# Kernel tuning notes

Hardware: AMD Instinct MI355X
Metric: run time of the kernel (lower is better)

The kernel has to match this reference:

```python
import jax, jax.numpy as jnp
import numpy as np

N = 100000      # nodes
E = 1600000     # edges (before self-loops)
F_IN = 128      # num_features
H = 4           # heads
C = 32          # out_channels per head (num_hidden)
SLOPE = 0.2     # leaky relu negative slope (alpha)


def setup_inputs() -> dict:
    key = jax.random.key(0)
    k = jax.random.split(key, 6)
    x = jax.random.normal(k[0], (N, F_IN), jnp.float32)
    edge_index = jax.random.randint(k[1], (2, E), 0, N, dtype=jnp.int64)
    W = jax.random.normal(k[2], (F_IN, H * C), jnp.float32) * (1.0 / np.sqrt(F_IN))
    att_src = jax.random.normal(k[3], (H, C), jnp.float32) * 0.1
    att_dst = jax.random.normal(k[4], (H, C), jnp.float32) * 0.1
    bias = jnp.zeros((H * C,), jnp.float32)
    return dict(x=x, W=W, att_src=att_src, att_dst=att_dst, bias=bias,
                edge_index=edge_index)


def reference(x, W, att_src, att_dst, bias, edge_index):
    # PyG GATConv (concat=True, add_self_loops=True), eval mode (dropout off).
    loops = jnp.arange(N, dtype=edge_index.dtype)
    ei = jnp.concatenate([edge_index, jnp.stack([loops, loops])], axis=1)
    src, dst = ei[0], ei[1]                     # [E+N]

    h = (x @ W).reshape(N, H, C)                # projected node features
    a_src = jnp.einsum('nhc,hc->nh', h, att_src)   # [N, H]
    a_dst = jnp.einsum('nhc,hc->nh', h, att_dst)   # [N, H]

    e = a_src[src] + a_dst[dst]                 # [E+N, H]
    e = jnp.where(e > 0, e, SLOPE * e)          # leaky relu

    # segment softmax over incoming edges of each dst node (per head)
    m = jax.lax.stop_gradient(jax.ops.segment_max(e, dst, num_segments=N))
    p = jnp.exp(e - m[dst])
    denom = jax.ops.segment_sum(p, dst, num_segments=N)
    alpha = p / (denom[dst] + 1e-16)            # [E+N, H]

    # weighted scatter-aggregate of source features
    out = jax.ops.segment_sum(alpha[:, :, None] * h[src], dst, num_segments=N)
    return out.reshape(N, H * C) + bias
```

## Files before the change

kernel.cpp:

```cpp
#include <hip/hip_runtime.h>
#include <hip/hip_bf16.h>
#include <math.h>

#define N_NODES 100000
#define F_IN    128
#define HC      128
#define NH      4
#define SLOPE   0.2f

#define PADK    136

#define NB      196
#define BSH     9
#define CAP     10240
#define CHUNK   2048
#define CURPAD  16

typedef __attribute__((ext_vector_type(8))) short short8;
typedef __attribute__((ext_vector_type(4))) float f32x4;
typedef __attribute__((ext_vector_type(2))) float fx2;

static __device__ __forceinline__ float leaky(float x) { return x > 0.f ? x : SLOPE * x; }

static __device__ __forceinline__ short f2bs(float f) {
    __hip_bfloat16 b = __float2bfloat16(f);
    return *reinterpret_cast<short*>(&b);
}

__global__ __launch_bounds__(256) void k_prep(const float* __restrict__ W,
                                              unsigned short* __restrict__ wt)
{
    int t = blockIdx.x * 256 + threadIdx.x;
    if (t < 128 * 128) {
        int k = t >> 7, n = t & 127;
        wt[n * 128 + k] = (unsigned short)f2bs(W[k * HC + n]);
    }
}

__global__ __launch_bounds__(256) void k_gemm(const float* __restrict__ x,
                                              const unsigned short* __restrict__ wt,
                                              const float* __restrict__ att_src,
                                              const float* __restrict__ att_dst,
                                              unsigned short* __restrict__ hb,
                                              float* __restrict__ a_src,
                                              float* __restrict__ a_dst)
{
    __shared__ short xs[64 * PADK];
    __shared__ short ws[128 * PADK];
    const int t  = threadIdx.x;
    const int r0 = blockIdx.x * 64;

    for (int i = t; i < 2048; i += 256) {
        int row = i >> 5, kq = (i & 31) * 4;
        int gr = r0 + row;
        float4 v = make_float4(0.f, 0.f, 0.f, 0.f);
        if (gr < N_NODES) v = ((const float4*)(x + (size_t)gr * F_IN))[i & 31];
        short* p = &xs[row * PADK + kq];
        p[0] = f2bs(v.x); p[1] = f2bs(v.y); p[2] = f2bs(v.z); p[3] = f2bs(v.w);
    }
    for (int i = t; i < 2048; i += 256) {
        int n = i >> 4, k0 = (i & 15) * 8;
        *(float4*)&ws[n * PADK + k0] = *(const float4*)&wt[n * 128 + k0];
    }
    __syncthreads();

    const int wave = t >> 6, lane = t & 63;
    const int quad = lane >> 4, l16 = lane & 15;
    const int wrow = wave * 16;

    f32x4 acc[8];
    #pragma unroll
    for (int nt = 0; nt < 8; ++nt) acc[nt] = (f32x4){0.f, 0.f, 0.f, 0.f};

    const short* ap = &xs[(wrow + l16) * PADK + quad * 8];
    #pragma unroll
    for (int kb = 0; kb < 4; ++kb) {
        short8 a = *(const short8*)(ap + kb * 32);
        #pragma unroll
        for (int nt = 0; nt < 8; ++nt) {
            short8 b = *(const short8*)&ws[(nt * 16 + l16) * PADK + kb * 32 + quad * 8];
            acc[nt] = __builtin_amdgcn_mfma_f32_16x16x32_bf16(a, b, acc[nt], 0, 0, 0);
        }
    }

    float att_s[8], att_d[8];
    #pragma unroll
    for (int nt = 0; nt < 8; ++nt) {
        att_s[nt] = att_src[nt * 16 + l16];
        att_d[nt] = att_dst[nt * 16 + l16];
    }

    #pragma unroll
    for (int g = 0; g < 4; ++g) {
        int r = r0 + wrow + quad * 4 + g;
        if (r < N_NODES) {
            #pragma unroll
            for (int nt = 0; nt < 8; ++nt)
                hb[(size_t)r * HC + nt * 16 + l16] = (unsigned short)f2bs(acc[nt][g]);
        }
        float s0 = acc[0][g] * att_s[0] + acc[1][g] * att_s[1];
        float s1 = acc[2][g] * att_s[2] + acc[3][g] * att_s[3];
        float s2 = acc[4][g] * att_s[4] + acc[5][g] * att_s[5];
        float s3 = acc[6][g] * att_s[6] + acc[7][g] * att_s[7];
        float d0 = acc[0][g] * att_d[0] + acc[1][g] * att_d[1];
        float d1 = acc[2][g] * att_d[2] + acc[3][g] * att_d[3];
        float d2 = acc[4][g] * att_d[4] + acc[5][g] * att_d[5];
        float d3 = acc[6][g] * att_d[6] + acc[7][g] * att_d[7];
        #pragma unroll
        for (int o = 1; o < 16; o <<= 1) {
            s0 += __shfl_xor(s0, o); s1 += __shfl_xor(s1, o);
            s2 += __shfl_xor(s2, o); s3 += __shfl_xor(s3, o);
            d0 += __shfl_xor(d0, o); d1 += __shfl_xor(d1, o);
            d2 += __shfl_xor(d2, o); d3 += __shfl_xor(d3, o);
        }
        if (l16 == 0 && r < N_NODES) {
            *(float4*)&a_src[r * NH] = make_float4(s0, s1, s2, s3);
            *(float4*)&a_dst[r * NH] = make_float4(d0, d1, d2, d3);
        }
    }
}

__global__ __launch_bounds__(256) void k_bucket(const int* __restrict__ srcp,
                                                const int* __restrict__ dstp,
                                                int* __restrict__ bucket_cursor,
                                                int* __restrict__ eb, int E)
{
    __shared__ int ebuf[CHUNK];
    __shared__ unsigned char bkt[CHUNK];
    __shared__ int hist[256];
    __shared__ int lexcl[257];
    __shared__ int gbase[256];
    __shared__ int sdata[256];

    const int t = threadIdx.x;
    const int base = blockIdx.x * CHUNK;

    hist[t] = 0;
    __syncthreads();

    #pragma unroll
    for (int j = 0; j < CHUNK / 256; ++j) {
        int i = base + t + j * 256;
        if (i < E) atomicAdd(&hist[dstp[i] >> BSH], 1);
    }
    __syncthreads();

    int cnt = hist[t];
    sdata[t] = cnt;
    __syncthreads();
    for (int o = 1; o < 256; o <<= 1) {
        int add = (t >= o) ? sdata[t - o] : 0;
        __syncthreads();
        sdata[t] += add;
        __syncthreads();
    }
    int excl = sdata[t] - cnt;
    lexcl[t] = excl;
    if (t == 255) lexcl[256] = sdata[255];
    hist[t] = excl;
    int gb = 0;
    if (t < NB && cnt > 0) gb = atomicAdd(&bucket_cursor[t * CURPAD], cnt);
    gbase[t] = t * CAP + gb;
    __syncthreads();

    #pragma unroll
    for (int j = 0; j < CHUNK / 256; ++j) {
        int i = base + t + j * 256;
        if (i < E) {
            int s = srcp[i], d = dstp[i];
            int b = d >> BSH;
            int r = atomicAdd(&hist[b], 1);
            ebuf[r] = (s << BSH) | (d & 511);
            bkt[r] = (unsigned char)b;
        }
    }
    __syncthreads();

    const int blockTotal = lexcl[256];
    for (int i = t; i < blockTotal; i += 256) {
        int b = bkt[i];
        eb[gbase[b] + (i - lexcl[b])] = ebuf[i];
    }
}

__global__ void k_bscan(const int* __restrict__ bucket_cursor,
                        int* __restrict__ bexcl)
{
    __shared__ int sdata[256];
    const int t = threadIdx.x;
    int nvalid = 0;
    if (t < NB) {
        int n0 = t * 512;
        nvalid = min(512, N_NODES - n0);
        if (nvalid < 0) nvalid = 0;
    }
    int v = (t < NB) ? bucket_cursor[t * CURPAD] + nvalid : 0;
    sdata[t] = v;
    __syncthreads();
    for (int o = 1; o < 256; o <<= 1) {
        int add = (t >= o) ? sdata[t - o] : 0;
        __syncthreads();
        sdata[t] += add;
        __syncthreads();
    }
    if (t < NB) bexcl[t] = sdata[t] - v;
}

__global__ __launch_bounds__(1024) void k_csr(const int* __restrict__ eb,
                                              const int* __restrict__ bucket_cursor,
                                              const int* __restrict__ bexcl,
                                              int* __restrict__ col,
                                              int2* __restrict__ rowse)
{
    __shared__ int deg[512];
    __shared__ int sdata[256];

    const int t  = threadIdx.x;
    const int b  = blockIdx.x;
    const int n0 = b * 512;
    const int cnt   = bucket_cursor[b * CURPAD];
    const int ebase = b * CAP;
    const int gofs  = bexcl[b];

    if (t < 512) deg[t] = (n0 + t < N_NODES) ? 1 : 0;
    __syncthreads();

    for (int i = t; i < cnt; i += 1024)
        atomicAdd(&deg[eb[ebase + i] & 511], 1);
    __syncthreads();

    int d0 = 0, d1 = 0, ps = 0;
    if (t < 256) {
        d0 = deg[2 * t]; d1 = deg[2 * t + 1];
        ps = d0 + d1;
        sdata[t] = ps;
    }
    __syncthreads();
    for (int o = 1; o < 256; o <<= 1) {
        int add = 0;
        if (t < 256 && t >= o) add = sdata[t - o];
        __syncthreads();
        if (t < 256) sdata[t] += add;
        __syncthreads();
    }
    if (t < 256) {
        int e0 = sdata[t] - ps;
        int e1 = e0 + d0;
        int na = n0 + 2 * t, nb2 = n0 + 2 * t + 1;
        if (na < N_NODES) {
            rowse[na] = make_int2(gofs + e0, gofs + e0 + d0);
            col[gofs + e0] = na;
        }
        if (nb2 < N_NODES) {
            rowse[nb2] = make_int2(gofs + e1, gofs + e1 + d1);
            col[gofs + e1] = nb2;
        }
        deg[2 * t]     = e0 + 1;
        deg[2 * t + 1] = e1 + 1;
    }
    __syncthreads();

    for (int i = t; i < cnt; i += 1024) {
        int v = eb[ebase + i];
        int r = atomicAdd(&deg[v & 511], 1);
        col[gofs + r] = v >> BSH;
    }
}

__global__ __launch_bounds__(256) void k_node(const unsigned short* __restrict__ hb,
                                              const float* __restrict__ a_src,
                                              const float* __restrict__ a_dst,
                                              const int2* __restrict__ rowse,
                                              const int* __restrict__ col,
                                              const float* __restrict__ bias,
                                              float* __restrict__ out)
{
    const int lane = threadIdx.x & 63;
    const int node = blockIdx.x * 4 + (threadIdx.x >> 6);
    if (node >= N_NODES) return;

    const int2 se = rowse[node];
    const int r0 = se.x, r1 = se.y;
    const int myh = lane >> 4;
    const float adm = a_dst[node * NH + myh];

    float denom = 0.f, acc0 = 0.f, acc1 = 0.f;
    int i = r0;
    for (; i + 8 <= r1; i += 8) {
        int s[8];
        #pragma unroll
        for (int j = 0; j < 8; ++j) s[j] = col[i + j];
        float as[8];
        #pragma unroll
        for (int j = 0; j < 8; ++j) as[j] = a_src[s[j] * NH + myh];
        unsigned int hv[8];
        #pragma unroll
        for (int j = 0; j < 8; ++j)
            hv[j] = *(const unsigned int*)&hb[(size_t)s[j] * HC + 2 * lane];
        #pragma unroll
        for (int j = 0; j < 8; ++j) {
            float p = __expf(leaky(as[j] + adm));
            denom += p;
            acc0 += p * __uint_as_float(hv[j] << 16);
            acc1 += p * __uint_as_float(hv[j] & 0xffff0000u);
        }
    }
    for (; i < r1; ++i) {
        int s = col[i];
        float p = __expf(leaky(a_src[s * NH + myh] + adm));
        unsigned int v = *(const unsigned int*)&hb[(size_t)s * HC + 2 * lane];
        denom += p;
        acc0 += p * __uint_as_float(v << 16);
        acc1 += p * __uint_as_float(v & 0xffff0000u);
    }

    float inv = 1.f / (denom + 1e-16f);
    fx2 o2;
    o2.x = acc0 * inv + bias[2 * lane];
    o2.y = acc1 * inv + bias[2 * lane + 1];
    __builtin_nontemporal_store(o2, (fx2*)&out[(size_t)node * HC + 2 * lane]);
}

extern "C" void kernel_launch(void* const* d_in, const int* in_sizes, int n_in,
                              void* d_out, int out_size, void* d_ws, size_t ws_size,
                              hipStream_t stream)
{
    const float* x       = (const float*)d_in[0];
    const float* W       = (const float*)d_in[1];
    const float* att_src = (const float*)d_in[2];
    const float* att_dst = (const float*)d_in[3];
    const float* bias    = (const float*)d_in[4];
    const int*   ei      = (const int*)d_in[5];
    const int E = in_sizes[5] / 2;
    const int* srcp = ei;
    const int* dstp = ei + E;
    float* out = (float*)d_out;

    char* wsb = (char*)d_ws;
    size_t off = 0;
    auto alloc = [&](size_t bytes) -> char* {
        char* p = wsb + off;
        off += (bytes + 255) & ~(size_t)255;
        return p;
    };
    unsigned short* hb = (unsigned short*)alloc((size_t)N_NODES * HC * sizeof(unsigned short));
    float* a_src   = (float*)alloc((size_t)N_NODES * NH * sizeof(float));
    float* a_dst   = (float*)alloc((size_t)N_NODES * NH * sizeof(float));
    int*   eb      = (int*)alloc((size_t)NB * CAP * sizeof(int));
    int*   col     = (int*)alloc((size_t)(E + N_NODES) * sizeof(int));
    int2*  rowse   = (int2*)alloc((size_t)N_NODES * sizeof(int2));
    int*   bcursor = (int*)alloc((size_t)NB * CURPAD * sizeof(int));
    int*   bexcl   = (int*)alloc(256 * sizeof(int));
    unsigned short* wt = (unsigned short*)alloc(128 * 128 * sizeof(unsigned short));

    (void)hipMemsetAsync(bcursor, 0, (size_t)NB * CURPAD * sizeof(int), stream);

    k_prep<<<64, 256, 0, stream>>>(W, wt);
    k_gemm<<<(N_NODES + 63) / 64, 256, 0, stream>>>(x, wt, att_src, att_dst,
                                                    hb, a_src, a_dst);
    k_bucket<<<(E + CHUNK - 1) / CHUNK, 256, 0, stream>>>(srcp, dstp, bcursor, eb, E);
    k_bscan<<<1, 256, 0, stream>>>(bcursor, bexcl);
    k_csr<<<NB, 1024, 0, stream>>>(eb, bcursor, bexcl, col, rowse);
    k_node<<<(N_NODES + 3) / 4, 256, 0, stream>>>(hb, a_src, a_dst, rowse, col, bias, out);
}
```

Before: 265.8 us.

## Merge GEMM and edge-bucketing kernels, drop memset and bucket scan

Result: faster. 251.0 us (-5.6%).

```diff
diff --git a/kernel.cpp b/kernel.cpp
--- a/kernel.cpp
+++ b/kernel.cpp
@@ -13,8 +13,11 @@
 #define NB      196
 #define BSH     9
 #define CAP     10240
+#define CAPC    10752
 #define CHUNK   2048
 #define CURPAD  16
+
+#define GEMM_BLOCKS 1563
 
 typedef __attribute__((ext_vector_type(8))) short short8;
 typedef __attribute__((ext_vector_type(4))) float f32x4;
@@ -27,188 +30,173 @@
     return *reinterpret_cast<short*>(&b);
 }
 
-__global__ __launch_bounds__(256) void k_prep(const float* __restrict__ W,
-                                              unsigned short* __restrict__ wt)
+__global__ __launch_bounds__(256) void k_pre(const float* __restrict__ W,
+                                             unsigned short* __restrict__ wt,
+                                             int* __restrict__ bucket_cursor)
 {
     int t = blockIdx.x * 256 + threadIdx.x;
     if (t < 128 * 128) {
         int k = t >> 7, n = t & 127;
         wt[n * 128 + k] = (unsigned short)f2bs(W[k * HC + n]);
     }
-}
-
-__global__ __launch_bounds__(256) void k_gemm(const float* __restrict__ x,
+    if (t < NB * CURPAD) bucket_cursor[t] = 0;
+}
+
+union SMem {
+    struct {
+        short xs[64 * PADK];
+        short ws[128 * PADK];
+    } g;
+    struct {
+        int ebuf[CHUNK];
+        unsigned char bkt[CHUNK];
+        int hist[256];
+        int lexcl[257];
+        int gbase[256];
+        int sdata[256];
+    } b;
+};
+
+__global__ __launch_bounds__(256) void k_main(const float* __restrict__ x,
                                               const unsigned short* __restrict__ wt,
                                               const float* __restrict__ att_src,
                                               const float* __restrict__ att_dst,
                                               unsigned short* __restrict__ hb,
                                               float* __restrict__ a_src,
-                                              float* __restrict__ a_dst)
-{
-    __shared__ short xs[64 * PADK];
-    __shared__ short ws[128 * PADK];
-    const int t  = threadIdx.x;
-    const int r0 = blockIdx.x * 64;
-
-    for (int i = t; i < 2048; i += 256) {
-        int row = i >> 5, kq = (i & 31) * 4;
-        int gr = r0 + row;
-        float4 v = make_float4(0.f, 0.f, 0.f, 0.f);
-        if (gr < N_NODES) v = ((const float4*)(x + (size_t)gr * F_IN))[i & 31];
-        short* p = &xs[row * PADK + kq];
-        p[0] = f2bs(v.x); p[1] = f2bs(v.y); p[2] = f2bs(v.z); p[3] = f2bs(v.w);
-    }
-    for (int i = t; i < 2048; i += 256) {
-        int n = i >> 4, k0 = (i & 15) * 8;
-        *(float4*)&ws[n * PADK + k0] = *(const float4*)&wt[n * 128 + k0];
-    }
-    __syncthreads();
-
-    const int wave = t >> 6, lane = t & 63;
-    const int quad = lane >> 4, l16 = lane & 15;
-    const int wrow = wave * 16;
-
-    f32x4 acc[8];
-    #pragma unroll
-    for (int nt = 0; nt < 8; ++nt) acc[nt] = (f32x4){0.f, 0.f, 0.f, 0.f};
-
-    const short* ap = &xs[(wrow + l16) * PADK + quad * 8];
-    #pragma unroll
-    for (int kb = 0; kb < 4; ++kb) {
-        short8 a = *(const short8*)(ap + kb * 32);
+                                              float* __restrict__ a_dst,
+                                              const int* __restrict__ srcp,
+                                              const int* __restrict__ dstp,
+                                              int* __restrict__ bucket_cursor,
+                                              int* __restrict__ eb, int E)
+{
+    __shared__ SMem sm;
+    const int t = threadIdx.x;
+
+    if (blockIdx.x < GEMM_BLOCKS) {
+        const int r0 = blockIdx.x * 64;
+
+        for (int i = t; i < 2048; i += 256) {
+            int row = i >> 5, kq = (i & 31) * 4;
+            int gr = r0 + row;
+            float4 v = make_float4(0.f, 0.f, 0.f, 0.f);
+            if (gr < N_NODES) v = ((const float4*)(x + (size_t)gr * F_IN))[i & 31];
+            short* p = &sm.g.xs[row * PADK + kq];
+            p[0] = f2bs(v.x); p[1] = f2bs(v.y); p[2] = f2bs(v.z); p[3] = f2bs(v.w);
+        }
+        for (int i = t; i < 2048; i += 256) {
+            int n = i >> 4, k0 = (i & 15) * 8;
+            *(float4*)&sm.g.ws[n * PADK + k0] = *(const float4*)&wt[n * 128 + k0];
+        }
+        __syncthreads();
+
+        const int wave = t >> 6, lane = t & 63;
+        const int quad = lane >> 4, l16 = lane & 15;
+        const int wrow = wave * 16;
+
+        f32x4 acc[8];
+        #pragma unroll
+        for (int nt = 0; nt < 8; ++nt) acc[nt] = (f32x4){0.f, 0.f, 0.f, 0.f};
+
+        const short* ap = &sm.g.xs[(wrow + l16) * PADK + quad * 8];
+        #pragma unroll
+        for (int kb = 0; kb < 4; ++kb) {
+            short8 a = *(const short8*)(ap + kb * 32);
+            #pragma unroll
+            for (int nt = 0; nt < 8; ++nt) {
+                short8 b = *(const short8*)&sm.g.ws[(nt * 16 + l16) * PADK + kb * 32 + quad * 8];
+                acc[nt] = __builtin_amdgcn_mfma_f32_16x16x32_bf16(a, b, acc[nt], 0, 0, 0);
+            }
+        }
+
+        float att_s[8], att_d[8];
         #pragma unroll
         for (int nt = 0; nt < 8; ++nt) {
-            short8 b = *(const short8*)&ws[(nt * 16 + l16) * PADK + kb * 32 + quad * 8];
-            acc[nt] = __builtin_amdgcn_mfma_f32_16x16x32_bf16(a, b, acc[nt], 0, 0, 0);
-        }
-    }
-
-    float att_s[8], att_d[8];
-    #pragma unroll
-    for (int nt = 0; nt < 8; ++nt) {
-        att_s[nt] = att_src[nt * 16 + l16];
-        att_d[nt] = att_dst[nt * 16 + l16];
-    }
-
-    #pragma unroll
-    for (int g = 0; g < 4; ++g) {
-        int r = r0 + wrow + quad * 4 + g;
-        if (r < N_NODES) {
+            att_s[nt] = att_src[nt * 16 + l16];
+            att_d[nt] = att_dst[nt * 16 + l16];
+        }
+
+        #pragma unroll
+        for (int g = 0; g < 4; ++g) {
+            int r = r0 + wrow + quad * 4 + g;
+            if (r < N_NODES) {
+                #pragma unroll
+                for (int nt = 0; nt < 8; ++nt)
+                    hb[(size_t)r * HC + nt * 16 + l16] = (unsigned short)f2bs(acc[nt][g]);
+            }
+            float s0 = acc[0][g] * att_s[0] + acc[1][g] * att_s[1];
+            float s1 = acc[2][g] * att_s[2] + acc[3][g] * att_s[3];
+            float s2 = acc[4][g] * att_s[4] + acc[5][g] * att_s[5];
+            float s3 = acc[6][g] * att_s[6] + acc[7][g] * att_s[7];
+            float d0 = acc[0][g] * att_d[0] + acc[1][g] * att_d[1];
+            float d1 = acc[2][g] * att_d[2] + acc[3][g] * att_d[3];
+            float d2 = acc[4][g] * att_d[4] + acc[5][g] * att_d[5];
+            float d3 = acc[6][g] * att_d[6] + acc[7][g] * att_d[7];
             #pragma unroll
-            for (int nt = 0; nt < 8; ++nt)
-                hb[(size_t)r * HC + nt * 16 + l16] = (unsigned short)f2bs(acc[nt][g]);
-        }
-        float s0 = acc[0][g] * att_s[0] + acc[1][g] * att_s[1];
-        float s1 = acc[2][g] * att_s[2] + acc[3][g] * att_s[3];
-        float s2 = acc[4][g] * att_s[4] + acc[5][g] * att_s[5];
-        float s3 = acc[6][g] * att_s[6] + acc[7][g] * att_s[7];
-        float d0 = acc[0][g] * att_d[0] + acc[1][g] * att_d[1];
-        float d1 = acc[2][g] * att_d[2] + acc[3][g] * att_d[3];
-        float d2 = acc[4][g] * att_d[4] + acc[5][g] * att_d[5];
-        float d3 = acc[6][g] * att_d[6] + acc[7][g] * att_d[7];
-        #pragma unroll
-        for (int o = 1; o < 16; o <<= 1) {
-            s0 += __shfl_xor(s0, o); s1 += __shfl_xor(s1, o);
-            s2 += __shfl_xor(s2, o); s3 += __shfl_xor(s3, o);
-            d0 += __shfl_xor(d0, o); d1 += __shfl_xor(d1, o);
-            d2 += __shfl_xor(d2, o); d3 += __shfl_xor(d3, o);
-        }
-        if (l16 == 0 && r < N_NODES) {
-            *(float4*)&a_src[r * NH] = make_float4(s0, s1, s2, s3);
-            *(float4*)&a_dst[r * NH] = make_float4(d0, d1, d2, d3);
-        }
-    }
-}
-
-__global__ __launch_bounds__(256) void k_bucket(const int* __restrict__ srcp,
-                                                const int* __restrict__ dstp,
-                                                int* __restrict__ bucket_cursor,
-                                                int* __restrict__ eb, int E)
-{
-    __shared__ int ebuf[CHUNK];
-    __shared__ unsigned char bkt[CHUNK];
-    __shared__ int hist[256];
-    __shared__ int lexcl[257];
-    __shared__ int gbase[256];
-    __shared__ int sdata[256];
-
-    const int t = threadIdx.x;
-    const int base = blockIdx.x * CHUNK;
-
-    hist[t] = 0;
-    __syncthreads();
-
-    #pragma unroll
-    for (int j = 0; j < CHUNK / 256; ++j) {
-        int i = base + t + j * 256;
-        if (i < E) atomicAdd(&hist[dstp[i] >> BSH], 1);
-    }
-    __syncthreads();
-
-    int cnt = hist[t];
-    sdata[t] = cnt;
-    __syncthreads();
-    for (int o = 1; o < 256; o <<= 1) {
-        int add = (t >= o) ? sdata[t - o] : 0;
-        __syncthreads();
-        sdata[t] += add;
-        __syncthreads();
-    }
-    int excl = sdata[t] - cnt;
-    lexcl[t] = excl;
-    if (t == 255) lexcl[256] = sdata[255];
-    hist[t] = excl;
-    int gb = 0;
-    if (t < NB && cnt > 0) gb = atomicAdd(&bucket_cursor[t * CURPAD], cnt);
-    gbase[t] = t * CAP + gb;
-    __syncthreads();
-
-    #pragma unroll
-    for (int j = 0; j < CHUNK / 256; ++j) {
-        int i = base + t + j * 256;
-        if (i < E) {
-            int s = srcp[i], d = dstp[i];
-            int b = d >> BSH;
-            int r = atomicAdd(&hist[b], 1);
-            ebuf[r] = (s << BSH) | (d & 511);
-            bkt[r] = (unsigned char)b;
-        }
-    }
-    __syncthreads();
-
-    const int blockTotal = lexcl[256];
-    for (int i = t; i < blockTotal; i += 256) {
-        int b = bkt[i];
-        eb[gbase[b] + (i - lexcl[b])] = ebuf[i];
-    }
-}
-
-__global__ void k_bscan(const int* __restrict__ bucket_cursor,
-                        int* __restrict__ bexcl)
-{
-    __shared__ int sdata[256];
-    const int t = threadIdx.x;
-    int nvalid = 0;
-    if (t < NB) {
-        int n0 = t * 512;
-        nvalid = min(512, N_NODES - n0);
-        if (nvalid < 0) nvalid = 0;
-    }
-    int v = (t < NB) ? bucket_cursor[t * CURPAD] + nvalid : 0;
-    sdata[t] = v;
-    __syncthreads();
-    for (int o = 1; o < 256; o <<= 1) {
-        int add = (t >= o) ? sdata[t - o] : 0;
-        __syncthreads();
-        sdata[t] += add;
-        __syncthreads();
-    }
-    if (t < NB) bexcl[t] = sdata[t] - v;
+            for (int o = 1; o < 16; o <<= 1) {
+                s0 += __shfl_xor(s0, o); s1 += __shfl_xor(s1, o);
+                s2 += __shfl_xor(s2, o); s3 += __shfl_xor(s3, o);
+                d0 += __shfl_xor(d0, o); d1 += __shfl_xor(d1, o);
+                d2 += __shfl_xor(d2, o); d3 += __shfl_xor(d3, o);
+            }
+            if (l16 == 0 && r < N_NODES) {
+                *(float4*)&a_src[r * NH] = make_float4(s0, s1, s2, s3);
+                *(float4*)&a_dst[r * NH] = make_float4(d0, d1, d2, d3);
+            }
+        }
+    } else {
+        const int base = (blockIdx.x - GEMM_BLOCKS) * CHUNK;
+
+        sm.b.hist[t] = 0;
+        __syncthreads();
+
+        #pragma unroll
+        for (int j = 0; j < CHUNK / 256; ++j) {
+            int i = base + t + j * 256;
+            if (i < E) atomicAdd(&sm.b.hist[dstp[i] >> BSH], 1);
+        }
+        __syncthreads();
+
+        int cnt = sm.b.hist[t];
+        sm.b.sdata[t] = cnt;
+        __syncthreads();
+        for (int o = 1; o < 256; o <<= 1) {
+            int add = (t >= o) ? sm.b.sdata[t - o] : 0;
+            __syncthreads();
+            sm.b.sdata[t] += add;
+            __syncthreads();
+        }
+        int excl = sm.b.sdata[t] - cnt;
+        sm.b.lexcl[t] = excl;
+        if (t == 255) sm.b.lexcl[256] = sm.b.sdata[255];
+        sm.b.hist[t] = excl;
+        int gb = 0;
+        if (t < NB && cnt > 0) gb = atomicAdd(&bucket_cursor[t * CURPAD], cnt);
+        sm.b.gbase[t] = t * CAP + gb;
+        __syncthreads();
+
+        #pragma unroll
+        for (int j = 0; j < CHUNK / 256; ++j) {
+            int i = base + t + j * 256;
+            if (i < E) {
+                int s = srcp[i], d = dstp[i];
+                int b = d >> BSH;
+                int r = atomicAdd(&sm.b.hist[b], 1);
+                sm.b.ebuf[r] = (s << BSH) | (d & 511);
+                sm.b.bkt[r] = (unsigned char)b;
+            }
+        }
+        __syncthreads();
+
+        const int blockTotal = sm.b.lexcl[256];
+        for (int i = t; i < blockTotal; i += 256) {
+            int b = sm.b.bkt[i];
+            eb[sm.b.gbase[b] + (i - sm.b.lexcl[b])] = sm.b.ebuf[i];
+        }
+    }
 }
 
 __global__ __launch_bounds__(1024) void k_csr(const int* __restrict__ eb,
                                               const int* __restrict__ bucket_cursor,
-                                              const int* __restrict__ bexcl,
                                               int* __restrict__ col,
                                               int2* __restrict__ rowse)
 {
@@ -220,7 +208,7 @@
     const int n0 = b * 512;
     const int cnt   = bucket_cursor[b * CURPAD];
     const int ebase = b * CAP;
-    const int gofs  = bexcl[b];
+    const int gofs  = b * CAPC;
 
     if (t < 512) deg[t] = (n0 + t < N_NODES) ? 1 : 0;
     __syncthreads();
@@ -347,19 +335,17 @@
     float* a_src   = (float*)alloc((size_t)N_NODES * NH * sizeof(float));
     float* a_dst   = (float*)alloc((size_t)N_NODES * NH * sizeof(float));
     int*   eb      = (int*)alloc((size_t)NB * CAP * sizeof(int));
-    int*   col     = (int*)alloc((size_t)(E + N_NODES) * sizeof(int));
+    int*   col     = (int*)alloc((size_t)NB * CAPC * sizeof(int));
     int2*  rowse   = (int2*)alloc((size_t)N_NODES * sizeof(int2));
     int*   bcursor = (int*)alloc((size_t)NB * CURPAD * sizeof(int));
-    int*   bexcl   = (int*)alloc(256 * sizeof(int));
     unsigned short* wt = (unsigned short*)alloc(128 * 128 * sizeof(unsigned short));
 
-    (void)hipMemsetAsync(bcursor, 0, (size_t)NB * CURPAD * sizeof(int), stream);
-
-    k_prep<<<64, 256, 0, stream>>>(W, wt);
-    k_gemm<<<(N_NODES + 63) / 64, 256, 0, stream>>>(x, wt, att_src, att_dst,
-                                                    hb, a_src, a_dst);
-    k_bucket<<<(E + CHUNK - 1) / CHUNK, 256, 0, stream>>>(srcp, dstp, bcursor, eb, E);
-    k_bscan<<<1, 256, 0, stream>>>(bcursor, bexcl);
-    k_csr<<<NB, 1024, 0, stream>>>(eb, bcursor, bexcl, col, rowse);
+    const int bucketBlocks = (E + CHUNK - 1) / CHUNK;
+
+    k_pre<<<64, 256, 0, stream>>>(W, wt, bcursor);
+    k_main<<<GEMM_BLOCKS + bucketBlocks, 256, 0, stream>>>(x, wt, att_src, att_dst,
+                                                           hb, a_src, a_dst,
+                                                           srcp, dstp, bcursor, eb, E);
+    k_csr<<<NB, 1024, 0, stream>>>(eb, bcursor, col, rowse);
     k_node<<<(N_NODES + 3) / 4, 256, 0, stream>>>(hb, a_src, a_dst, rowse, col, bias, out);
 }
```
